# Kernel optimization log

Measured on AMD Instinct MI355X. Metric: run time of the kernel, lower is better.

## Reference

```python
import jax, jax.numpy as jnp
import numpy as np

B, L, D = 32, 256, 1024
ALIGN = 1024
FF = 2048
NUM_CLASSES = 3


def setup_inputs() -> dict:
    key = jax.random.key(0)
    ks = jax.random.split(key, 10)
    u = lambda k, shape: jax.random.uniform(k, shape, jnp.float32, -1.0, 1.0)
    return {
        "premises": jax.random.normal(ks[0], (B, L, D), jnp.float32),
        "hypotheses": jax.random.normal(ks[1], (B, L, D), jnp.float32),
        "W_F": u(ks[2], (D, ALIGN)),
        "W_G": u(ks[3], (2 * D, FF)),
        "W1": u(ks[4], (2 * FF, FF)) * 0.02,
        "b1": jnp.zeros((FF,), jnp.float32),
        "W2": u(ks[5], (FF, FF)) * 0.02,
        "b2": jnp.zeros((FF,), jnp.float32),
        "W3": u(ks[6], (FF, NUM_CLASSES)) * 0.02,
        "b3": jnp.zeros((NUM_CLASSES,), jnp.float32),
    }


def reference(premises, hypotheses, W_F, W_G, W1, b1, W2, b2, W3, b3):
    # ---- align: tanh-projected cross attention ----
    F_p = jnp.tanh(jnp.einsum("bpd,da->bpa", premises, W_F))      # [B,Lp,A]
    F_h = jnp.tanh(jnp.einsum("bhd,da->bha", hypotheses, W_F))    # [B,Lh,A]
    eijs = jnp.einsum("bpa,bha->bph", F_p, F_h)                   # [B,Lp,Lh]
    attn = jax.nn.softmax(eijs, axis=-1)                          # tf.nn.softmax: last axis
    betas = jnp.einsum("bph,bhd->bpd", attn, hypotheses)          # [B,Lp,D]
    alphas = jnp.einsum("bph,bpd->bhd", attn, premises)           # [B,Lh,D]

    # ---- compare (dropout is identity: p_keep = 1.0 at eval) ----
    V1 = jnp.tanh(jnp.concatenate([premises, betas], axis=2) @ W_G)    # [B,Lp,FF]
    V2 = jnp.tanh(jnp.concatenate([hypotheses, alphas], axis=2) @ W_G) # [B,Lh,FF]

    # ---- aggregate: sum-pool over sequence, concat ----
    agg = jnp.concatenate([V1.sum(axis=1), V2.sum(axis=1)], axis=1)    # [B,2*FF]

    # ---- classifier MLP ----
    a1 = jnp.tanh(agg @ W1 + b1)
    a2 = jnp.tanh(a1 @ W2 + b2)
    logits = a2 @ W3 + b3                                              # [B,3]
    return logits
```

## Files before the change

### kernel.cpp

```cpp
#include <hip/hip_runtime.h>
#include <hip/hip_bf16.h>
#include <stdint.h>


typedef __attribute__((ext_vector_type(8))) short    short8_t;
typedef __attribute__((ext_vector_type(4))) float    float4_t;
typedef __attribute__((ext_vector_type(8))) _Float16 half8_t;
typedef __attribute__((ext_vector_type(4))) _Float16 half4_t;

#define DEVI static __device__ __forceinline__

DEVI short f2bf(float f) {
  union { float f; unsigned u; } v; v.f = f;
  unsigned r = v.u + 0x7fffu + ((v.u >> 16) & 1u);
  return (short)(r >> 16);
}
DEVI float bf2f(short s) {
  union { unsigned u; float f; } v;
  v.u = ((unsigned)(unsigned short)s) << 16;
  return v.f;
}
DEVI void split2(float x, short& hi, short& lo) {
  hi = f2bf(x);
  lo = f2bf(x - bf2f(hi));
}
DEVI float fast_tanh(float x) {
  float e = __expf(2.0f * x);
  return 1.0f - 2.0f / (e + 1.0f);
}
DEVI void gload16(const void* g, void* l) {
  __builtin_amdgcn_global_load_lds(
      (const __attribute__((address_space(1))) void*)g,
      (__attribute__((address_space(3))) void*)l, 16, 0, 0);
}

template <int DO_TANH, int OUT_MODE>
__global__ __launch_bounds__(256) void gemm_nt_split(
    const short* __restrict__ Ah, const short* __restrict__ Al, int lda, long sA,
    const short* __restrict__ Bh, const short* __restrict__ Bl, int ldb, long sB,
    void* __restrict__ Ch, void* __restrict__ Cl, int ldc, long sC,
    int M, int K, int kslices)
{
  __shared__ __align__(16) short Ash[128 * 32];
  __shared__ __align__(16) short Asl[128 * 32];
  __shared__ __align__(16) short Bsh[128 * 32];
  __shared__ __align__(16) short Bsl[128 * 32];

  const int z  = blockIdx.z;
  const int zb = z / kslices;
  const int zk = z - zb * kslices;
  const int Ksub = K / kslices;
  const int kbeg = zk * Ksub, kend = kbeg + Ksub;

  Ah += (size_t)zb * sA;  Al += (size_t)zb * sA;
  Bh += (size_t)zb * sB;  Bl += (size_t)zb * sB;

  const int row0 = blockIdx.x * 128;
  const int col0 = blockIdx.y * 128;

  const int t    = threadIdx.x;
  const int lane = t & 63;
  const int wave = t >> 6;
  const int wr = wave >> 1, wc = wave & 1;
  const int m15 = lane & 15, q = lane >> 4;

  const int schk = ((t & 3) ^ ((t >> 3) & 3)) * 8;
  const short* pAh = Ah + (size_t)(row0 + (t >> 2)) * lda + kbeg + schk;
  const short* pAl = Al + (size_t)(row0 + (t >> 2)) * lda + kbeg + schk;
  const short* pBh = Bh + (size_t)(col0 + (t >> 2)) * ldb + kbeg + schk;
  const short* pBl = Bl + (size_t)(col0 + (t >> 2)) * ldb + kbeg + schk;
  const size_t a64 = (size_t)64 * lda, b64 = (size_t)64 * ldb;
  short* lAh = &Ash[wave * 512];
  short* lAl = &Asl[wave * 512];
  short* lBh = &Bsh[wave * 512];
  short* lBl = &Bsl[wave * 512];

  const int fs2 = (q ^ ((m15 >> 1) & 3)) * 8;

  float4_t acc[4][4];
#pragma unroll
  for (int i = 0; i < 4; ++i)
#pragma unroll
    for (int j = 0; j < 4; ++j) acc[i][j] = (float4_t)0.0f;

  for (int k0 = kbeg; k0 < kend; k0 += 32) {
    gload16(pAh, lAh);  gload16(pAh + a64, lAh + 2048);
    gload16(pAl, lAl);  gload16(pAl + a64, lAl + 2048);
    gload16(pBh, lBh);  gload16(pBh + b64, lBh + 2048);
    gload16(pBl, lBl);  gload16(pBl + b64, lBl + 2048);
    pAh += 32; pAl += 32; pBh += 32; pBl += 32;
    __syncthreads();

    short8_t ah[4], al[4];
#pragma unroll
    for (int i = 0; i < 4; ++i) {
      const int ra = (wr * 64 + i * 16 + m15) * 32 + fs2;
      ah[i] = *(const short8_t*)&Ash[ra];
      al[i] = *(const short8_t*)&Asl[ra];
    }
#pragma unroll
    for (int j = 0; j < 4; ++j) {
      const int rb = (wc * 64 + j * 16 + m15) * 32 + fs2;
      short8_t bh = *(const short8_t*)&Bsh[rb];
      short8_t bl = *(const short8_t*)&Bsl[rb];
#pragma unroll
      for (int i = 0; i < 4; ++i) {
        acc[i][j] = __builtin_amdgcn_mfma_f32_16x16x32_bf16(ah[i], bh, acc[i][j], 0, 0, 0);
        acc[i][j] = __builtin_amdgcn_mfma_f32_16x16x32_bf16(ah[i], bl, acc[i][j], 0, 0, 0);
        acc[i][j] = __builtin_amdgcn_mfma_f32_16x16x32_bf16(al[i], bh, acc[i][j], 0, 0, 0);
      }
    }
    __syncthreads();
  }

  short* Chs = (short*)Ch + (size_t)zb * sC;
  short* Cls = (short*)Cl + (size_t)zb * sC;
  float* Cf  = (float*)Ch + (size_t)zb * sC;
#pragma unroll
  for (int i = 0; i < 4; ++i) {
#pragma unroll
    for (int r = 0; r < 4; ++r) {
      int gm = row0 + wr * 64 + i * 16 + q * 4 + r;
      if (gm < M) {
#pragma unroll
        for (int j = 0; j < 4; ++j) {
          int gn = col0 + wc * 64 + j * 16 + m15;
          float v = acc[i][j][r];
          if (DO_TANH) v = fast_tanh(v);
          if (OUT_MODE == 0) {
            atomicAdd(&Cf[(size_t)gm * ldc + gn], v);
          } else {
            short hi, lo; split2(v, hi, lo);
            Chs[(size_t)gm * ldc + gn] = hi;
            Cls[(size_t)gm * ldc + gn] = lo;
          }
        }
      }
    }
  }
}

template <int MODE>
__global__ __launch_bounds__(256) void gemm_f16(
    const _Float16* __restrict__ A, int lda, long sA,
    const _Float16* __restrict__ B, int ldb, long sB,
    _Float16* __restrict__ C, int ldc, long sC,
    int K, float* __restrict__ agg)
{
  __shared__ __align__(16) _Float16 As[2 * 128 * 32];
  __shared__ __align__(16) _Float16 Bs[2 * 128 * 32];

  const int z = blockIdx.z;
  A += (size_t)z * sA;
  B += (size_t)z * sB;

  const int row0 = blockIdx.x * 128;
  const int col0 = blockIdx.y * 128;
  const int t = threadIdx.x, lane = t & 63, wave = t >> 6;
  const int wr = wave >> 1, wc = wave & 1;
  const int m15 = lane & 15, q = lane >> 4;

  const int srow = wave * 32 + (lane >> 2);
  const int cg   = ((lane & 3) ^ ((lane >> 3) & 3)) * 8;
  const _Float16* gA0 = A + (size_t)(row0 + srow) * lda + cg;
  const _Float16* gA1 = gA0 + (size_t)16 * lda;
  const _Float16* gB0 = B + (size_t)(col0 + srow) * ldb + cg;
  const _Float16* gB1 = gB0 + (size_t)16 * ldb;
  const _Float16* gA0b = gA0 + 32;
  const _Float16* gA1b = gA1 + 32;
  const _Float16* gB0b = gB0 + 32;
  const _Float16* gB1b = gB1 + 32;
  _Float16* lA0  = &As[(wave * 32) * 32];
  _Float16* lA1  = &As[(wave * 32 + 16) * 32];
  _Float16* lB0  = &Bs[(wave * 32) * 32];
  _Float16* lB1  = &Bs[(wave * 32 + 16) * 32];
  _Float16* lA0b = lA0 + 4096;
  _Float16* lA1b = lA1 + 4096;
  _Float16* lB0b = lB0 + 4096;
  _Float16* lB1b = lB1 + 4096;

  const int fs = (q ^ ((m15 >> 1) & 3)) * 8;
  int aoff[4], boff[4];
#pragma unroll
  for (int i = 0; i < 4; ++i) {
    aoff[i] = (wr * 64 + i * 16 + m15) * 32 + fs;
    boff[i] = (wc * 64 + i * 16 + m15) * 32 + fs;
  }

  float4_t acc[4][4];
#pragma unroll
  for (int i = 0; i < 4; ++i)
#pragma unroll
    for (int j = 0; j < 4; ++j) acc[i][j] = (float4_t)0.0f;

  for (int k0 = 0; k0 < K; k0 += 64) {
    gload16(gA0, lA0);  gload16(gA1, lA1);
    gload16(gB0, lB0);  gload16(gB1, lB1);
    gload16(gA0b, lA0b); gload16(gA1b, lA1b);
    gload16(gB0b, lB0b); gload16(gB1b, lB1b);
    gA0 += 64; gA1 += 64; gB0 += 64; gB1 += 64;
    gA0b += 64; gA1b += 64; gB0b += 64; gB1b += 64;
    __syncthreads();

#pragma unroll
    for (int h = 0; h < 2; ++h) {
      half8_t af[4], bfr[4];
#pragma unroll
      for (int i = 0; i < 4; ++i) af[i]  = *(const half8_t*)&As[h * 4096 + aoff[i]];
#pragma unroll
      for (int j = 0; j < 4; ++j) bfr[j] = *(const half8_t*)&Bs[h * 4096 + boff[j]];
#pragma unroll
      for (int i = 0; i < 4; ++i)
#pragma unroll
        for (int j = 0; j < 4; ++j)
          acc[i][j] = __builtin_amdgcn_mfma_f32_16x16x32_f16(af[i], bfr[j], acc[i][j], 0, 0, 0);
    }
    __syncthreads();
  }

  {
    _Float16* Cp = C + (size_t)z * sC;
#pragma unroll
    for (int i = 0; i < 4; ++i)
#pragma unroll
      for (int r = 0; r < 4; ++r) {
        int gm = row0 + wr * 64 + i * 16 + q * 4 + r;
#pragma unroll
        for (int j = 0; j < 4; ++j) {
          int gn = col0 + wc * 64 + j * 16 + m15;
          Cp[(size_t)gm * ldc + gn] = (_Float16)acc[i][j][r];
        }
      }
  }
}

__global__ __launch_bounds__(512, 2) void gemm_f16_sum8(
    const _Float16* __restrict__ A, int lda,
    const _Float16* __restrict__ B, int ldb,
    int K, float* __restrict__ agg)
{
  __shared__ __align__(16) _Float16 LDS[4][2 * 256 * 32];

  const int row0 = blockIdx.x * 256;
  const int col0 = blockIdx.y * 256;
  const int tid  = threadIdx.x;
  const int lane = tid & 63, wave = tid >> 6;
  const int wr = wave >> 2, wc = wave & 3;
  const int m15 = lane & 15, q = lane >> 4;
  const int nt = K / 32;

  const int srow = wave * 32 + (lane >> 2);
  const int cg   = ((lane & 3) ^ ((lane >> 3) & 3)) * 8;
  const _Float16* gA = A + (size_t)(row0 + srow) * lda + cg;
  const _Float16* gB = B + (size_t)(col0 + srow) * ldb + cg;

  auto stageA = [&](int t) {
    const _Float16* g = gA + t * 32;
    _Float16* l = &LDS[t & 3][wave * 1024];
    gload16(g, l);
    gload16(g + (size_t)16 * lda, l + 512);
  };
  auto stageB = [&](int t) {
    const _Float16* g = gB + t * 32;
    _Float16* l = &LDS[t & 3][8192 + wave * 1024];
    gload16(g, l);
    gload16(g + (size_t)16 * ldb, l + 512);
  };

  const int xq = (q ^ ((m15 >> 1) & 3)) * 8;
  int aoff[8], boff[4];
#pragma unroll
  for (int i = 0; i < 8; ++i)
    aoff[i] = (wr * 128 + i * 16 + m15) * 32 + xq;
#pragma unroll
  for (int j = 0; j < 4; ++j)
    boff[j] = 8192 + (wc * 64 + j * 16 + m15) * 32 + xq;

  float4_t acc[8][4];
#pragma unroll
  for (int i = 0; i < 8; ++i)
#pragma unroll
    for (int j = 0; j < 4; ++j) acc[i][j] = (float4_t)0.0f;

  stageA(0); stageB(0);
  stageA(1); stageB(1);
  asm volatile("s_waitcnt vmcnt(4)");
  __builtin_amdgcn_s_barrier();

  for (int t = 0; t < nt; ++t) {
    const _Float16* buf = &LDS[t & 3][0];
    __builtin_amdgcn_sched_barrier(0);

    half8_t a0[4], a1[4], bb[4];
#pragma unroll
    for (int i = 0; i < 4; ++i) a0[i] = *(const half8_t*)&buf[aoff[i]];
#pragma unroll
    for (int j = 0; j < 4; ++j) bb[j] = *(const half8_t*)&buf[boff[j]];
#pragma unroll
    for (int i = 0; i < 4; ++i) a1[i] = *(const half8_t*)&buf[aoff[4 + i]];

    if (t + 2 < nt) { stageA(t + 2); stageB(t + 2); }

    __builtin_amdgcn_s_setprio(1);
#pragma unroll
    for (int i = 0; i < 4; ++i)
#pragma unroll
      for (int j = 0; j < 4; ++j)
        acc[i][j] = __builtin_amdgcn_mfma_f32_16x16x32_f16(a0[i], bb[j], acc[i][j], 0, 0, 0);
#pragma unroll
    for (int i = 0; i < 4; ++i)
#pragma unroll
      for (int j = 0; j < 4; ++j)
        acc[4 + i][j] = __builtin_amdgcn_mfma_f32_16x16x32_f16(a1[i], bb[j], acc[4 + i][j], 0, 0, 0);
    __builtin_amdgcn_s_setprio(0);

    __builtin_amdgcn_sched_barrier(0);
    if (t + 2 < nt) {
      asm volatile("s_waitcnt vmcnt(4)");
    } else if (t + 1 < nt) {
      asm volatile("s_waitcnt vmcnt(0)");
    }
    __builtin_amdgcn_s_barrier();
  }

  const int half_ = row0 >= 8192;
  const int b     = (row0 & 8191) >> 8;
#pragma unroll
  for (int j = 0; j < 4; ++j) {
    float s = 0.0f;
#pragma unroll
    for (int i = 0; i < 8; ++i)
#pragma unroll
      for (int r = 0; r < 4; ++r) s += fast_tanh(acc[i][j][r]);
    s += __shfl_xor(s, 16);
    s += __shfl_xor(s, 32);
    if (q == 0) {
      int col = col0 + wc * 64 + j * 16 + m15;
      atomicAdd(&agg[(size_t)b * 4096 + half_ * 2048 + col], s);
    }
  }
}

__global__ __launch_bounds__(256) void transpose_split(
    const float* __restrict__ in, short* __restrict__ oh, short* __restrict__ ol,
    int R, int C)
{
  __shared__ float tile[32][33];
  const int tx = threadIdx.x & 31, ty = threadIdx.x >> 5;
  const int c0 = blockIdx.x * 32, r0 = blockIdx.y * 32;
#pragma unroll
  for (int i = 0; i < 4; ++i) {
    int r = ty + i * 8;
    tile[r][tx] = in[(size_t)(r0 + r) * C + c0 + tx];
  }
  __syncthreads();
#pragma unroll
  for (int i = 0; i < 4; ++i) {
    int cc = ty + i * 8;
    float v = tile[tx][cc];
    short hi, lo; split2(v, hi, lo);
    size_t o = (size_t)(c0 + cc) * R + r0 + tx;
    oh[o] = hi;
    ol[o] = lo;
  }
}

__global__ __launch_bounds__(256) void transpose_f16(
    const float* __restrict__ in, _Float16* __restrict__ out, int R, int C)
{
  __shared__ float tile[32][33];
  const int tx = threadIdx.x & 31, ty = threadIdx.x >> 5;
  const int c0 = blockIdx.x * 32, r0 = blockIdx.y * 32;
#pragma unroll
  for (int i = 0; i < 4; ++i) {
    int r = ty + i * 8;
    tile[r][tx] = in[(size_t)(r0 + r) * C + c0 + tx];
  }
  __syncthreads();
#pragma unroll
  for (int i = 0; i < 4; ++i) {
    int cc = ty + i * 8;
    out[(size_t)(c0 + cc) * R + r0 + tx] = (_Float16)tile[tx][cc];
  }
}

__global__ __launch_bounds__(256) void transpose_f16_ph(
    const float* __restrict__ P, const float* __restrict__ Hh,
    _Float16* __restrict__ out)
{
  __shared__ float tile[32][33];
  const int zz = blockIdx.z;
  const float* in = (zz < 32 ? P : Hh) + (size_t)(zz & 31) * (256 * 1024);
  _Float16* o = out + (size_t)zz * (1024 * 256);
  const int tx = threadIdx.x & 31, ty = threadIdx.x >> 5;
  const int c0 = blockIdx.x * 32, r0 = blockIdx.y * 32;
#pragma unroll
  for (int i = 0; i < 4; ++i) {
    int r = ty + i * 8;
    tile[r][tx] = in[(size_t)(r0 + r) * 1024 + c0 + tx];
  }
  __syncthreads();
#pragma unroll
  for (int i = 0; i < 4; ++i) {
    int cc = ty + i * 8;
    o[(size_t)(c0 + cc) * 256 + r0 + tx] = (_Float16)tile[tx][cc];
  }
}

__global__ __launch_bounds__(256) void transpose_b2b(
    const short* __restrict__ in, short* __restrict__ out,
    int R, int C, long sIn, long sOut)
{
  __shared__ short tile[32][33];
  in  += (size_t)blockIdx.z * sIn;
  out += (size_t)blockIdx.z * sOut;
  const int tx = threadIdx.x & 31, ty = threadIdx.x >> 5;
  const int c0 = blockIdx.x * 32, r0 = blockIdx.y * 32;
#pragma unroll
  for (int i = 0; i < 4; ++i) {
    int r = ty + i * 8;
    tile[r][tx] = in[(size_t)(r0 + r) * C + c0 + tx];
  }
  __syncthreads();
#pragma unroll
  for (int i = 0; i < 4; ++i) {
    int cc = ty + i * 8;
    out[(size_t)(c0 + cc) * R + r0 + tx] = tile[tx][cc];
  }
}

__global__ __launch_bounds__(256) void conv_in(
    const float* __restrict__ P, const float* __restrict__ Hh,
    short* __restrict__ oh, short* __restrict__ ol, _Float16* __restrict__ cat)
{
  const int zz = blockIdx.z;
  const float* in = zz ? Hh : P;
  oh  += (size_t)zz * 8192 * 1024;
  ol  += (size_t)zz * 8192 * 1024;
  cat += (size_t)zz * 8192 * 2048;
  size_t i = ((size_t)blockIdx.x * 256 + threadIdx.x) * 4;
  float4 v = *(const float4*)&in[i];
  short4 h, l;
  split2(v.x, h.x, l.x); split2(v.y, h.y, l.y);
  split2(v.z, h.z, l.z); split2(v.w, h.w, l.w);
  *(short4*)&oh[i] = h;
  *(short4*)&ol[i] = l;
  size_t row = i >> 10;
  int col    = (int)(i & 1023);
  half4_t c16;
  c16.x = (_Float16)v.x; c16.y = (_Float16)v.y;
  c16.z = (_Float16)v.z; c16.w = (_Float16)v.w;
  *(half4_t*)&cat[row * 2048 + col] = c16;
}

__global__ __launch_bounds__(256) void conv_split(
    const float* __restrict__ in, short* __restrict__ oh, short* __restrict__ ol,
    int n)
{
  int i = (blockIdx.x * 256 + threadIdx.x) * 4;
  if (i < n) {
    float4 v = *(const float4*)&in[i];
    short4 h, l;
    split2(v.x, h.x, l.x); split2(v.y, h.y, l.y);
    split2(v.z, h.z, l.z); split2(v.w, h.w, l.w);
    *(short4*)&oh[i] = h;
    *(short4*)&ol[i] = l;
  }
}

__global__ __launch_bounds__(256) void zero_f32(float* __restrict__ p, int n)
{
  int i = blockIdx.x * 256 + threadIdx.x;
  if (i < n) p[i] = 0.0f;
}

__global__ __launch_bounds__(256) void softmax_rows(
    const float* __restrict__ e, _Float16* __restrict__ attn)
{
  const int row  = blockIdx.x * 4 + (threadIdx.x >> 6);
  const int lane = threadIdx.x & 63;
  const float4 v = *(const float4*)&e[(size_t)row * 256 + lane * 4];
  float m = fmaxf(fmaxf(v.x, v.y), fmaxf(v.z, v.w));
#pragma unroll
  for (int off = 32; off; off >>= 1) m = fmaxf(m, __shfl_xor(m, off));
  float e0 = __expf(v.x - m), e1 = __expf(v.y - m);
  float e2 = __expf(v.z - m), e3 = __expf(v.w - m);
  float s = e0 + e1 + e2 + e3;
#pragma unroll
  for (int off = 32; off; off >>= 1) s += __shfl_xor(s, off);
  float inv = 1.0f / s;
  half4_t o;
  o.x = (_Float16)(e0 * inv); o.y = (_Float16)(e1 * inv);
  o.z = (_Float16)(e2 * inv); o.w = (_Float16)(e3 * inv);
  *(half4_t*)&attn[(size_t)row * 256 + lane * 4] = o;
}

__global__ __launch_bounds__(256) void bias_tanh_split(
    const float* __restrict__ c, const float* __restrict__ bias,
    short* __restrict__ oh, short* __restrict__ ol, int n)
{
  int i = blockIdx.x * 256 + threadIdx.x;
  if (i < n) {
    float v = fast_tanh(c[i] + bias[i & 2047]);
    short hi, lo; split2(v, hi, lo);
    oh[i] = hi;
    ol[i] = lo;
  }
}

__global__ __launch_bounds__(256) void logits2(
    const float* __restrict__ c2f, const float* __restrict__ b2,
    const float* __restrict__ W3, const float* __restrict__ b3,
    float* __restrict__ out)
{
  const int b = blockIdx.x, t = threadIdx.x;
  float p0 = 0.f, p1 = 0.f, p2 = 0.f;
  for (int k = t; k < 2048; k += 256) {
    float a = fast_tanh(c2f[b * 2048 + k] + b2[k]);
    p0 += a * W3[k * 3 + 0];
    p1 += a * W3[k * 3 + 1];
    p2 += a * W3[k * 3 + 2];
  }
#pragma unroll
  for (int off = 32; off; off >>= 1) {
    p0 += __shfl_xor(p0, off);
    p1 += __shfl_xor(p1, off);
    p2 += __shfl_xor(p2, off);
  }
  __shared__ float red[4][3];
  if ((t & 63) == 0) {
    red[t >> 6][0] = p0; red[t >> 6][1] = p1; red[t >> 6][2] = p2;
  }
  __syncthreads();
  if (t < 3) out[b * 3 + t] = b3[t] + red[0][t] + red[1][t] + red[2][t] + red[3][t];
}

extern "C" void kernel_launch(void* const* d_in, const int* in_sizes, int n_in,
                              void* d_out, int out_size, void* d_ws, size_t ws_size,
                              hipStream_t stream) {
  (void)in_sizes; (void)n_in; (void)out_size; (void)ws_size;
  const float* P   = (const float*)d_in[0];
  const float* H   = (const float*)d_in[1];
  const float* W_F = (const float*)d_in[2];
  const float* W_G = (const float*)d_in[3];
  const float* W1  = (const float*)d_in[4];
  const float* b1  = (const float*)d_in[5];
  const float* W2  = (const float*)d_in[6];
  const float* b2  = (const float*)d_in[7];
  const float* W3  = (const float*)d_in[8];
  const float* b3  = (const float*)d_in[9];
  float* out = (float*)d_out;

  char* wsp = (char*)d_ws;
  auto alloc = [&](size_t bytes) {
    char* p = wsp;
    wsp += (bytes + 255) & ~(size_t)255;
    return p;
  };
  short*    Pp_h  = (short*)alloc(16384ull * 1024 * 2);
  short*    Pp_l  = (short*)alloc(16384ull * 1024 * 2);
  _Float16* Cat16 = (_Float16*)alloc(16384ull * 2048 * 2);
  short*    Fbuf  = (short*)alloc(32ull * 1024 * 1024 * 2);
  short*    WFT_h = (short*)alloc(1024ull * 1024 * 2);
  short*    WFT_l = (short*)alloc(1024ull * 1024 * 2);
  _Float16* WGT16 = (_Float16*)alloc(2048ull * 2048 * 2);
  float*    eijs  = (float*)alloc(32ull * 256 * 256 * 4);
  _Float16* attn  = (_Float16*)alloc(32ull * 256 * 256 * 2);
  _Float16* attnT = (_Float16*)alloc(32ull * 256 * 256 * 2);
  float*    agg   = (float*)alloc(32ull * 4096 * 4);
  short*    aggb_h= (short*)alloc(128ull * 4096 * 2);
  short*    aggb_l= (short*)alloc(128ull * 4096 * 2);
  float*    c1f   = (float*)alloc(32ull * 2048 * 4);
  float*    c2f   = (float*)alloc(32ull * 2048 * 4);
  short*    a1_h  = (short*)alloc(128ull * 2048 * 2);
  short*    a1_l  = (short*)alloc(128ull * 2048 * 2);

  short* F_h = Fbuf;
  short* F_l = Fbuf + 16384ull * 1024;
  _Float16* PHbT = (_Float16*)Fbuf;
  _Float16* PbT  = PHbT;
  _Float16* HbT  = PHbT + 32ull * 1024 * 256;
  short* W1T_h = Fbuf;
  short* W1T_l = Fbuf +  8ull * 1024 * 1024;
  short* W2T_h = Fbuf + 16ull * 1024 * 1024;
  short* W2T_l = Fbuf + 20ull * 1024 * 1024;

  conv_in<<<dim3(8192, 1, 2), 256, 0, stream>>>(P, H, Pp_h, Pp_l, Cat16);
  transpose_split<<<dim3(32, 32, 1), 256, 0, stream>>>(W_F, WFT_h, WFT_l, 1024, 1024);
  transpose_f16<<<dim3(64, 64, 1), 256, 0, stream>>>(W_G, WGT16, 2048, 2048);

  gemm_nt_split<1, 1><<<dim3(128, 8, 1), 256, 0, stream>>>(
      Pp_h, Pp_l, 1024, 0, WFT_h, WFT_l, 1024, 0,
      F_h, F_l, 1024, 0, 16384, 1024, 1);

  zero_f32<<<8192, 256, 0, stream>>>(eijs, 32 * 256 * 256);
  gemm_nt_split<0, 0><<<dim3(2, 2, 128), 256, 0, stream>>>(
      F_h, F_l, 1024, 256 * 1024,
      F_h + 8192ull * 1024, F_l + 8192ull * 1024, 1024, 256 * 1024,
      eijs, nullptr, 256, 65536, 256, 1024, 4);

  softmax_rows<<<2048, 256, 0, stream>>>(eijs, attn);
  transpose_b2b<<<dim3(8, 8, 32), 256, 0, stream>>>(
      (const short*)attn, (short*)attnT, 256, 256, 65536, 65536);
  transpose_f16_ph<<<dim3(32, 8, 64), 256, 0, stream>>>(P, H, PHbT);

  gemm_f16<1><<<dim3(2, 8, 32), 256, 0, stream>>>(
      attn, 256, 65536, HbT, 256, 1024 * 256,
      Cat16 + 1024, 2048, 256 * 2048, 256, nullptr);
  gemm_f16<1><<<dim3(2, 8, 32), 256, 0, stream>>>(
      attnT, 256, 65536, PbT, 256, 1024 * 256,
      Cat16 + 8192ull * 2048 + 1024, 2048, 256 * 2048, 256, nullptr);

  zero_f32<<<512, 256, 0, stream>>>(agg, 32 * 4096);
  gemm_f16_sum8<<<dim3(64, 8, 1), 512, 0, stream>>>(
      Cat16, 2048, WGT16, 2048, 2048, agg);

  transpose_split<<<dim3(64, 128, 1), 256, 0, stream>>>(W1, W1T_h, W1T_l, 4096, 2048);
  transpose_split<<<dim3(64, 64, 1),  256, 0, stream>>>(W2, W2T_h, W2T_l, 2048, 2048);
  conv_split<<<128, 256, 0, stream>>>(agg, aggb_h, aggb_l, 32 * 4096);
  zero_f32<<<256, 256, 0, stream>>>(c1f, 32 * 2048);
  gemm_nt_split<0, 0><<<dim3(1, 16, 8), 256, 0, stream>>>(
      aggb_h, aggb_l, 4096, 0, W1T_h, W1T_l, 4096, 0,
      c1f, nullptr, 2048, 0, 32, 4096, 8);
  bias_tanh_split<<<256, 256, 0, stream>>>(c1f, b1, a1_h, a1_l, 32 * 2048);
  zero_f32<<<256, 256, 0, stream>>>(c2f, 32 * 2048);
  gemm_nt_split<0, 0><<<dim3(1, 16, 4), 256, 0, stream>>>(
      a1_h, a1_l, 2048, 0, W2T_h, W2T_l, 2048, 0,
      c2f, nullptr, 2048, 0, 32, 2048, 4);
  logits2<<<32, 256, 0, stream>>>(c2f, b2, W3, b3, out);
}
```

Measured before the change: 591.5 us.

## Fuse input conversion with transpose, merge alignment GEMMs, use fp32 skinny MLP GEMMs

Input conversion (bf16 hi/lo split plus fp16 concat copy) is fused with the fp16 transpose of P/H into a single kernel, so the separate transpose pass is gone. The two attention-weighted GEMMs become one launch, with an XOR on the batch index picking the other operand. The classifier MLP drops the W1/W2 transposes, the hi/lo splits and the split-bf16 MFMA GEMMs in favour of a simple fp32 skinny GEMM that reads the weights directly. The split-K factor for the eijs GEMM is halved. The CUDA-core skinny GEMM could be slower per FLOP, but it removes several transpose and convert passes over the large weights.

New measurement: 600.6 us. About the same (+1.5%).

```diff
diff --git a/kernel.cpp b/kernel.cpp
--- a/kernel.cpp
+++ b/kernel.cpp
@@ -140,19 +140,18 @@
   }
 }
 
-template <int MODE>
 __global__ __launch_bounds__(256) void gemm_f16(
     const _Float16* __restrict__ A, int lda, long sA,
     const _Float16* __restrict__ B, int ldb, long sB,
     _Float16* __restrict__ C, int ldc, long sC,
-    int K, float* __restrict__ agg)
+    int K, int bxor)
 {
   __shared__ __align__(16) _Float16 As[2 * 128 * 32];
   __shared__ __align__(16) _Float16 Bs[2 * 128 * 32];
 
   const int z = blockIdx.z;
   A += (size_t)z * sA;
-  B += (size_t)z * sB;
+  B += (size_t)(z ^ bxor) * sB;
 
   const int row0 = blockIdx.x * 128;
   const int col0 = blockIdx.y * 128;
@@ -384,29 +383,6 @@
   }
 }
 
-__global__ __launch_bounds__(256) void transpose_f16_ph(
-    const float* __restrict__ P, const float* __restrict__ Hh,
-    _Float16* __restrict__ out)
-{
-  __shared__ float tile[32][33];
-  const int zz = blockIdx.z;
-  const float* in = (zz < 32 ? P : Hh) + (size_t)(zz & 31) * (256 * 1024);
-  _Float16* o = out + (size_t)zz * (1024 * 256);
-  const int tx = threadIdx.x & 31, ty = threadIdx.x >> 5;
-  const int c0 = blockIdx.x * 32, r0 = blockIdx.y * 32;
-#pragma unroll
-  for (int i = 0; i < 4; ++i) {
-    int r = ty + i * 8;
-    tile[r][tx] = in[(size_t)(r0 + r) * 1024 + c0 + tx];
-  }
-  __syncthreads();
-#pragma unroll
-  for (int i = 0; i < 4; ++i) {
-    int cc = ty + i * 8;
-    o[(size_t)(c0 + cc) * 256 + r0 + tx] = (_Float16)tile[tx][cc];
-  }
-}
-
 __global__ __launch_bounds__(256) void transpose_b2b(
     const short* __restrict__ in, short* __restrict__ out,
     int R, int C, long sIn, long sOut)
@@ -429,42 +405,37 @@
   }
 }
 
-__global__ __launch_bounds__(256) void conv_in(
+__global__ __launch_bounds__(256) void conv_in_t(
     const float* __restrict__ P, const float* __restrict__ Hh,
-    short* __restrict__ oh, short* __restrict__ ol, _Float16* __restrict__ cat)
-{
-  const int zz = blockIdx.z;
-  const float* in = zz ? Hh : P;
-  oh  += (size_t)zz * 8192 * 1024;
-  ol  += (size_t)zz * 8192 * 1024;
-  cat += (size_t)zz * 8192 * 2048;
-  size_t i = ((size_t)blockIdx.x * 256 + threadIdx.x) * 4;
-  float4 v = *(const float4*)&in[i];
-  short4 h, l;
-  split2(v.x, h.x, l.x); split2(v.y, h.y, l.y);
-  split2(v.z, h.z, l.z); split2(v.w, h.w, l.w);
-  *(short4*)&oh[i] = h;
-  *(short4*)&ol[i] = l;
-  size_t row = i >> 10;
-  int col    = (int)(i & 1023);
-  half4_t c16;
-  c16.x = (_Float16)v.x; c16.y = (_Float16)v.y;
-  c16.z = (_Float16)v.z; c16.w = (_Float16)v.w;
-  *(half4_t*)&cat[row * 2048 + col] = c16;
-}
-
-__global__ __launch_bounds__(256) void conv_split(
-    const float* __restrict__ in, short* __restrict__ oh, short* __restrict__ ol,
-    int n)
-{
-  int i = (blockIdx.x * 256 + threadIdx.x) * 4;
-  if (i < n) {
-    float4 v = *(const float4*)&in[i];
-    short4 h, l;
-    split2(v.x, h.x, l.x); split2(v.y, h.y, l.y);
-    split2(v.z, h.z, l.z); split2(v.w, h.w, l.w);
-    *(short4*)&oh[i] = h;
-    *(short4*)&ol[i] = l;
+    short* __restrict__ oh, short* __restrict__ ol,
+    _Float16* __restrict__ cat, _Float16* __restrict__ phbt)
+{
+  __shared__ float tile[32][33];
+  const int zb   = blockIdx.z;
+  const int half = zb >> 5;
+  const int b    = zb & 31;
+  const float* in = (half ? Hh : P) + (size_t)b * 256 * 1024;
+  const int c0 = blockIdx.x * 32;
+  const int r0 = blockIdx.y * 32;
+  const int tx = threadIdx.x & 31, ty = threadIdx.x >> 5;
+  const size_t rowbase = (size_t)half * 8192 + (size_t)b * 256;
+#pragma unroll
+  for (int i = 0; i < 4; ++i) {
+    int r = ty + i * 8;
+    float v = in[(size_t)(r0 + r) * 1024 + c0 + tx];
+    tile[r][tx] = v;
+    short hi, lo; split2(v, hi, lo);
+    size_t o = (rowbase + r0 + r) * 1024 + c0 + tx;
+    oh[o] = hi;
+    ol[o] = lo;
+    cat[(rowbase + r0 + r) * 2048 + c0 + tx] = (_Float16)v;
+  }
+  __syncthreads();
+  _Float16* op = phbt + (size_t)zb * 1024 * 256;
+#pragma unroll
+  for (int i = 0; i < 4; ++i) {
+    int cc = ty + i * 8;
+    op[(size_t)(c0 + cc) * 256 + r0 + tx] = (_Float16)tile[tx][cc];
   }
 }
 
@@ -495,17 +466,40 @@
   *(half4_t*)&attn[(size_t)row * 256 + lane * 4] = o;
 }
 
-__global__ __launch_bounds__(256) void bias_tanh_split(
+__global__ __launch_bounds__(256) void skinny_gemm(
+    const float* __restrict__ A, const float* __restrict__ B,
+    float* __restrict__ out, int N, int K)
+{
+  __shared__ float Asl[32][256];
+  const int n0 = blockIdx.x * 64;
+  const int k0 = blockIdx.y * 256;
+  const int t  = threadIdx.x;
+  for (int i = t; i < 32 * 256; i += 256) {
+    int m = i >> 8, k = i & 255;
+    Asl[m][k] = A[(size_t)m * K + k0 + k];
+  }
+  __syncthreads();
+  const int l = t & 63, w = t >> 6;
+  const int n = n0 + l;
+  float acc[8] = {0.f, 0.f, 0.f, 0.f, 0.f, 0.f, 0.f, 0.f};
+  const float* Bp = B + (size_t)k0 * N + n;
+  for (int k = 0; k < 256; ++k) {
+    float bv = Bp[(size_t)k * N];
+#pragma unroll
+    for (int m = 0; m < 8; ++m)
+      acc[m] += Asl[w * 8 + m][k] * bv;
+  }
+#pragma unroll
+  for (int m = 0; m < 8; ++m)
+    atomicAdd(&out[(size_t)(w * 8 + m) * N + n], acc[m]);
+}
+
+__global__ __launch_bounds__(256) void bias_tanh_f32(
     const float* __restrict__ c, const float* __restrict__ bias,
-    short* __restrict__ oh, short* __restrict__ ol, int n)
+    float* __restrict__ o, int n)
 {
   int i = blockIdx.x * 256 + threadIdx.x;
-  if (i < n) {
-    float v = fast_tanh(c[i] + bias[i & 2047]);
-    short hi, lo; split2(v, hi, lo);
-    oh[i] = hi;
-    ol[i] = lo;
-  }
+  if (i < n) o[i] = fast_tanh(c[i] + bias[i & 2047]);
 }
 
 __global__ __launch_bounds__(256) void logits2(
@@ -561,6 +555,7 @@
   short*    Pp_l  = (short*)alloc(16384ull * 1024 * 2);
   _Float16* Cat16 = (_Float16*)alloc(16384ull * 2048 * 2);
   short*    Fbuf  = (short*)alloc(32ull * 1024 * 1024 * 2);
+  _Float16* PHbT  = (_Float16*)alloc(64ull * 1024 * 256 * 2);
   short*    WFT_h = (short*)alloc(1024ull * 1024 * 2);
   short*    WFT_l = (short*)alloc(1024ull * 1024 * 2);
   _Float16* WGT16 = (_Float16*)alloc(2048ull * 2048 * 2);
@@ -568,24 +563,14 @@
   _Float16* attn  = (_Float16*)alloc(32ull * 256 * 256 * 2);
   _Float16* attnT = (_Float16*)alloc(32ull * 256 * 256 * 2);
   float*    agg   = (float*)alloc(32ull * 4096 * 4);
-  short*    aggb_h= (short*)alloc(128ull * 4096 * 2);
-  short*    aggb_l= (short*)alloc(128ull * 4096 * 2);
   float*    c1f   = (float*)alloc(32ull * 2048 * 4);
   float*    c2f   = (float*)alloc(32ull * 2048 * 4);
-  short*    a1_h  = (short*)alloc(128ull * 2048 * 2);
-  short*    a1_l  = (short*)alloc(128ull * 2048 * 2);
+  float*    a1f   = (float*)alloc(32ull * 2048 * 4);
 
   short* F_h = Fbuf;
   short* F_l = Fbuf + 16384ull * 1024;
-  _Float16* PHbT = (_Float16*)Fbuf;
-  _Float16* PbT  = PHbT;
-  _Float16* HbT  = PHbT + 32ull * 1024 * 256;
-  short* W1T_h = Fbuf;
-  short* W1T_l = Fbuf +  8ull * 1024 * 1024;
-  short* W2T_h = Fbuf + 16ull * 1024 * 1024;
-  short* W2T_l = Fbuf + 20ull * 1024 * 1024;
-
-  conv_in<<<dim3(8192, 1, 2), 256, 0, stream>>>(P, H, Pp_h, Pp_l, Cat16);
+
+  conv_in_t<<<dim3(32, 8, 64), 256, 0, stream>>>(P, H, Pp_h, Pp_l, Cat16, PHbT);
   transpose_split<<<dim3(32, 32, 1), 256, 0, stream>>>(W_F, WFT_h, WFT_l, 1024, 1024);
   transpose_f16<<<dim3(64, 64, 1), 256, 0, stream>>>(W_G, WGT16, 2048, 2048);
 
@@ -594,38 +579,27 @@
       F_h, F_l, 1024, 0, 16384, 1024, 1);
 
   zero_f32<<<8192, 256, 0, stream>>>(eijs, 32 * 256 * 256);
-  gemm_nt_split<0, 0><<<dim3(2, 2, 128), 256, 0, stream>>>(
+  gemm_nt_split<0, 0><<<dim3(2, 2, 64), 256, 0, stream>>>(
       F_h, F_l, 1024, 256 * 1024,
       F_h + 8192ull * 1024, F_l + 8192ull * 1024, 1024, 256 * 1024,
-      eijs, nullptr, 256, 65536, 256, 1024, 4);
+      eijs, nullptr, 256, 65536, 256, 1024, 2);
 
   softmax_rows<<<2048, 256, 0, stream>>>(eijs, attn);
   transpose_b2b<<<dim3(8, 8, 32), 256, 0, stream>>>(
       (const short*)attn, (short*)attnT, 256, 256, 65536, 65536);
-  transpose_f16_ph<<<dim3(32, 8, 64), 256, 0, stream>>>(P, H, PHbT);
-
-  gemm_f16<1><<<dim3(2, 8, 32), 256, 0, stream>>>(
-      attn, 256, 65536, HbT, 256, 1024 * 256,
-      Cat16 + 1024, 2048, 256 * 2048, 256, nullptr);
-  gemm_f16<1><<<dim3(2, 8, 32), 256, 0, stream>>>(
-      attnT, 256, 65536, PbT, 256, 1024 * 256,
-      Cat16 + 8192ull * 2048 + 1024, 2048, 256 * 2048, 256, nullptr);
+
+  gemm_f16<<<dim3(2, 8, 64), 256, 0, stream>>>(
+      attn, 256, 65536, PHbT, 256, 1024 * 256,
+      Cat16 + 1024, 2048, 256 * 2048, 256, 32);
 
   zero_f32<<<512, 256, 0, stream>>>(agg, 32 * 4096);
   gemm_f16_sum8<<<dim3(64, 8, 1), 512, 0, stream>>>(
       Cat16, 2048, WGT16, 2048, 2048, agg);
 
-  transpose_split<<<dim3(64, 128, 1), 256, 0, stream>>>(W1, W1T_h, W1T_l, 4096, 2048);
-  transpose_split<<<dim3(64, 64, 1),  256, 0, stream>>>(W2, W2T_h, W2T_l, 2048, 2048);
-  conv_split<<<128, 256, 0, stream>>>(agg, aggb_h, aggb_l, 32 * 4096);
   zero_f32<<<256, 256, 0, stream>>>(c1f, 32 * 2048);
-  gemm_nt_split<0, 0><<<dim3(1, 16, 8), 256, 0, stream>>>(
-      aggb_h, aggb_l, 4096, 0, W1T_h, W1T_l, 4096, 0,
-      c1f, nullptr, 2048, 0, 32, 4096, 8);
-  bias_tanh_split<<<256, 256, 0, stream>>>(c1f, b1, a1_h, a1_l, 32 * 2048);
+  skinny_gemm<<<dim3(32, 16), 256, 0, stream>>>(agg, W1, c1f, 2048, 4096);
+  bias_tanh_f32<<<256, 256, 0, stream>>>(c1f, b1, a1f, 32 * 2048);
   zero_f32<<<256, 256, 0, stream>>>(c2f, 32 * 2048);
-  gemm_nt_split<0, 0><<<dim3(1, 16, 4), 256, 0, stream>>>(
-      a1_h, a1_l, 2048, 0, W2T_h, W2T_l, 2048, 0,
-      c2f, nullptr, 2048, 0, 32, 2048, 4);
+  skinny_gemm<<<dim3(32, 8), 256, 0, stream>>>(a1f, W2, c2f, 2048, 2048);
   logits2<<<32, 256, 0, stream>>>(c2f, b2, W3, b3, out);
 }
```
